# Kernel tuning notes

Measured on AMD Instinct MI355X. Metric: run time of the kernel, lower is better.

Reference implementation:

```python
import jax, jax.numpy as jnp
import numpy as np
import math

B, S, E, H = 2, 2048, 1024, 16
D = E // H  # d_head = 64

def setup_inputs() -> dict:
    key = jax.random.key(0)
    ks = jax.random.split(key, 7)
    query = jax.random.normal(ks[0], (B, S, E), dtype=jnp.float32)
    k_in = jax.random.normal(ks[1], (B, S, E), dtype=jnp.float32)
    v_in = jax.random.normal(ks[2], (B, S, E), dtype=jnp.float32)
    # causal mask, broadcastable over batch and heads; mask==0 positions are blocked
    mask = jnp.tril(jnp.ones((S, S), dtype=jnp.int32))[None, None]
    scale = 1.0 / math.sqrt(E)
    w_q = jax.random.normal(ks[3], (E, E), dtype=jnp.float32) * scale
    w_k = jax.random.normal(ks[4], (E, E), dtype=jnp.float32) * scale
    w_v = jax.random.normal(ks[5], (E, E), dtype=jnp.float32) * scale
    w_o = jax.random.normal(ks[6], (E, E), dtype=jnp.float32) * scale
    return {"query": query, "key": k_in, "value": v_in, "mask": mask,
            "w_q": w_q, "w_k": w_k, "w_v": w_v, "w_o": w_o}

def reference(query, key, value, mask, w_q, w_k, w_v, w_o):
    # projections (nn.Linear with no bias: x @ W^T); split heads -> [B,H,S,D]
    q = (query @ w_q.T).reshape(B, S, H, D).transpose(0, 2, 1, 3)
    k = (key @ w_k.T).reshape(B, S, H, D).transpose(0, 2, 1, 3)
    v = (value @ w_v.T).reshape(B, S, H, D).transpose(0, 2, 1, 3)
    # scaled dot-product scores [B,H,S,S]
    scores = jnp.einsum('bhqd,bhkd->bhqk', q, k) / math.sqrt(D)
    scores = jnp.where(mask == 0, jnp.float32(-1e9), scores)
    attn = jax.nn.softmax(scores, axis=-1)  # dropout p=0.0 -> identity
    out = jnp.einsum('bhqk,bhkd->bhqd', attn, v)  # [B,H,S,D]
    out = out.transpose(0, 2, 1, 3).reshape(B, S, E)
    return out @ w_o.T
```

## Files before the change

### kernel.cpp

```cpp
#include <hip/hip_runtime.h>
#include <hip/hip_bf16.h>

#define B_ 2
#define S_ 2048
#define E_ 1024
#define H_ 16
#define D_ 64

typedef __attribute__((ext_vector_type(8))) short bf16x8;
typedef __attribute__((ext_vector_type(4))) float f32x4;

static __device__ __forceinline__ unsigned short f2bf(float x) {
    union { float f; unsigned u; } v; v.f = x;
    unsigned r = v.u + 0x7FFF + ((v.u >> 16) & 1);
    return (unsigned short)(r >> 16);
}

static __device__ __forceinline__ unsigned pack2bf(float a, float b) {
    union { float f; unsigned u; } x, y; x.f = a; y.f = b;
    unsigned ra = x.u + 0x7FFF + ((x.u >> 16) & 1);
    unsigned rb = y.u + 0x7FFF + ((y.u >> 16) & 1);
    return (ra >> 16) | (rb & 0xFFFF0000u);
}

static __device__ __forceinline__ unsigned packtrunc(float a, float b) {
    union { float f; unsigned u; } x, y; x.f = a; y.f = b;
    return __builtin_amdgcn_perm(y.u, x.u, 0x07060302);
}

static __device__ __forceinline__ void async_copy16(const void* gsrc, void* ldst) {
    __builtin_amdgcn_global_load_lds(
        (const __attribute__((address_space(1))) void*)gsrc,
        (__attribute__((address_space(3))) void*)ldst, 16, 0, 0);
}

__global__ void cvt_multi(const float* __restrict__ s0, const float* __restrict__ s1,
                          const float* __restrict__ s2, const float* __restrict__ s3,
                          unsigned short* __restrict__ dst, int n4,
                          float c0, float c1, float c2, float c3) {
    const float* src = (blockIdx.y == 0) ? s0 : (blockIdx.y == 1) ? s1
                     : (blockIdx.y == 2) ? s2 : s3;
    float c = (blockIdx.y == 0) ? c0 : (blockIdx.y == 1) ? c1
            : (blockIdx.y == 2) ? c2 : c3;
    int i = blockIdx.x * blockDim.x + threadIdx.x;
    if (i >= n4) return;
    float4 f = ((const float4*)src)[i];
    ushort4 o;
    o.x = f2bf(f.x * c); o.y = f2bf(f.y * c); o.z = f2bf(f.z * c); o.w = f2bf(f.w * c);
    ((ushort4*)(dst + (size_t)blockIdx.y * n4 * 4))[i] = o;
}

template <int MODE>
__global__ __launch_bounds__(256) void gemm128(
    const unsigned short* __restrict__ A0, const unsigned short* __restrict__ B0,
    void* __restrict__ C0, int M, int N, int K) {
    __shared__ __align__(16) unsigned short Al[2][128 * 64];
    __shared__ __align__(16) unsigned short Bl[2][128 * 64];
    const unsigned short* A = A0;
    const unsigned short* Bm = B0;
    int z = 0;
    if (MODE == 4) {
        z = blockIdx.z;
        A  = A0 + (size_t)z * 4194304;
        Bm = B0 + (size_t)z * 1048576;
    }
    const int bm = blockIdx.y * 128, bn = blockIdx.x * 128;
    const int tid = threadIdx.x;
    const int w = tid >> 6, lane = tid & 63;
    const int col = lane & 15, quad = lane >> 4, swz = col & 7;
    const int wm = (w >> 1) * 64, wn = (w & 1) * 64;

    f32x4 acc[4][4] = {};

#pragma unroll
    for (int it = 0; it < 4; it++) {
        int s = tid + it * 256, r = s >> 3, cg = (s & 7) ^ (r & 7);
        async_copy16(A + (size_t)(bm + r) * K + cg * 8, &Al[0][s * 8]);
        async_copy16(Bm + (size_t)(bn + r) * K + cg * 8, &Bl[0][s * 8]);
    }

    const int nk = K >> 6;
    for (int kt = 0; kt < nk; kt++) {
        const int cur = kt & 1;
        __syncthreads();
        if (kt + 1 < nk) {
            const int k1 = (kt + 1) << 6, nb = cur ^ 1;
#pragma unroll
            for (int it = 0; it < 4; it++) {
                int s = tid + it * 256, r = s >> 3, cg = (s & 7) ^ (r & 7);
                async_copy16(A + (size_t)(bm + r) * K + k1 + cg * 8, &Al[nb][s * 8]);
                async_copy16(Bm + (size_t)(bn + r) * K + k1 + cg * 8, &Bl[nb][s * 8]);
            }
        }
        const unsigned short* Ab = &Al[cur][0];
        const unsigned short* Bb = &Bl[cur][0];
#pragma unroll
        for (int h = 0; h < 2; h++) {
            const int cq = ((h * 4 + quad) ^ swz) * 8;
            bf16x8 af[4], bf[4];
#pragma unroll
            for (int i = 0; i < 4; i++) af[i] = *(const bf16x8*)&Ab[(wm + i * 16 + col) * 64 + cq];
#pragma unroll
            for (int j = 0; j < 4; j++) bf[j] = *(const bf16x8*)&Bb[(wn + j * 16 + col) * 64 + cq];
#pragma unroll
            for (int i = 0; i < 4; i++)
#pragma unroll
                for (int j = 0; j < 4; j++)
                    acc[i][j] = __builtin_amdgcn_mfma_f32_16x16x32_bf16(af[i], bf[j], acc[i][j], 0, 0, 0);
        }
    }

    if (MODE == 3) {
#pragma unroll
        for (int i = 0; i < 4; i++)
#pragma unroll
            for (int j = 0; j < 4; j++)
#pragma unroll
                for (int r = 0; r < 4; r++) {
                    int gm = bm + wm + i * 16 + quad * 4 + r;
                    int gn = bn + wn + j * 16 + col;
                    ((float*)C0)[(size_t)gm * N + gn] = acc[i][j][r];
                }
    } else {
        __syncthreads();
        unsigned short* scr = ((w < 2) ? &Al[0][0] : &Bl[0][0]) + (w & 1) * 4096;
        const int b  = (bm + wm) >> 11;
        const int s0 = (bm + wm) & 2047;
        const int hh = (bn + wn) >> 6;
        unsigned short* outp = (unsigned short*)C0 + (size_t)z * 4194304;
        if (z == 2) {
#pragma unroll
            for (int i = 0; i < 4; i++)
#pragma unroll
                for (int j = 0; j < 4; j++) {
                    int n = j * 16 + col;
                    int c = i * 2 + (quad >> 1);
                    uint2 pk;
                    pk.x = pack2bf(acc[i][j][0], acc[i][j][1]);
                    pk.y = pack2bf(acc[i][j][2], acc[i][j][3]);
                    *(uint2*)&scr[n * 64 + ((c ^ (n & 7)) << 3) + ((quad & 1) << 2)] = pk;
                }
#pragma unroll
            for (int it = 0; it < 8; it++) {
                int slot = it * 64 + lane, n = slot >> 3, c = slot & 7;
                uint4 v = *(uint4*)&scr[n * 64 + ((c ^ (n & 7)) << 3)];
                *(uint4*)&outp[(((size_t)b * H_ + hh) * D_ + n) * S_ + s0 + c * 8] = v;
            }
        } else {
#pragma unroll
            for (int i = 0; i < 4; i++)
#pragma unroll
                for (int j = 0; j < 4; j++)
#pragma unroll
                    for (int r = 0; r < 4; r++) {
                        int m = i * 16 + quad * 4 + r, n = j * 16 + col;
                        scr[m * 64 + (((n >> 3) ^ (m & 7)) << 3) + (n & 7)] = f2bf(acc[i][j][r]);
                    }
#pragma unroll
            for (int it = 0; it < 8; it++) {
                int slot = it * 64 + lane, m = slot >> 3, c = slot & 7;
                uint4 v = *(uint4*)&scr[m * 64 + ((c ^ (m & 7)) << 3)];
                *(uint4*)&outp[(((size_t)b * H_ + hh) * S_ + s0 + m) * (size_t)D_ + c * 8] = v;
            }
        }
    }
}

__global__ __launch_bounds__(512) void attn_kernel(
    const unsigned short* __restrict__ Q, const unsigned short* __restrict__ K_,
    const unsigned short* __restrict__ Vt, unsigned short* __restrict__ Out) {
    __shared__ __align__(16) unsigned short KV[4][4096];
    __shared__ __align__(16) float Lred[4][2][64];
    const int bh = blockIdx.y;
    const int qb = (bh >= 16) ? (int)blockIdx.x : 15 - (int)blockIdx.x;
    const int q0 = qb * 128;
    const int tid = threadIdx.x;
    const int w = tid >> 6, lane = tid & 63;
    const int qg = w >> 1, kh = w & 1, kh32 = kh << 5;
    const int col = lane & 15, quad = lane >> 4, swz = col & 7;
    const int qw0 = q0 + qg * 32;
    const float NINF = -__builtin_huge_valf();

    const unsigned short* Qh = Q + (size_t)bh * S_ * D_;
    const unsigned short* Kh = K_ + (size_t)bh * S_ * D_;
    const unsigned short* Vh = Vt + (size_t)bh * D_ * S_;

    bf16x8 qf[2][2];
#pragma unroll
    for (int i = 0; i < 2; i++)
#pragma unroll
        for (int h = 0; h < 2; h++)
            qf[i][h] = *(const bf16x8*)(Qh + (size_t)(qw0 + i * 16 + col) * 64 + h * 32 + quad * 8);

    f32x4 o[2][4] = {};
    float lsum[2] = {0.f, 0.f};

    {
        int s = tid, r = s >> 3, cg = (s & 7) ^ (r & 7);
        async_copy16(Kh + (size_t)r * 64 + cg * 8, &KV[0][s * 8]);
        async_copy16(Vh + (size_t)r * S_ + cg * 8, &KV[2][s * 8]);
    }

    const int nk = 2 * (qb + 1);
    for (int kt = 0; kt < nk; kt++) {
        const int k0 = kt * 64;
        const int cur = kt & 1;
        __syncthreads();
        if (kt + 1 < nk) {
            const int k1 = k0 + 64, nb = cur ^ 1;
            int s = tid, r = s >> 3, cg = (s & 7) ^ (r & 7);
            async_copy16(Kh + (size_t)(k1 + r) * 64 + cg * 8, &KV[nb][s * 8]);
            async_copy16(Vh + (size_t)r * S_ + k1 + cg * 8, &KV[2 + nb][s * 8]);
        }
        if (k0 + kh32 > qw0 + 31) continue;

        const unsigned short* Kb = &KV[cur][0];
        const unsigned short* Vb = &KV[2 + cur][0];

        f32x4 sc[2][2] = {};
#pragma unroll
        for (int h = 0; h < 2; h++) {
            const int cq = ((h * 4 + quad) ^ swz) * 8;
#pragma unroll
            for (int ct = 0; ct < 2; ct++) {
                bf16x8 kf = *(const bf16x8*)&Kb[(kh32 + ct * 16 + col) * 64 + cq];
                sc[0][ct] = __builtin_amdgcn_mfma_f32_16x16x32_bf16(kf, qf[0][h], sc[0][ct], 0, 0, 0);
                sc[1][ct] = __builtin_amdgcn_mfma_f32_16x16x32_bf16(kf, qf[1][h], sc[1][ct], 0, 0, 0);
            }
        }
        if (k0 + kh32 + 31 <= qw0) {
#pragma unroll
            for (int i = 0; i < 2; i++)
#pragma unroll
                for (int ct = 0; ct < 2; ct++) {
#pragma unroll
                    for (int r = 0; r < 4; r++)
                        sc[i][ct][r] = __builtin_amdgcn_exp2f(sc[i][ct][r]);
                    lsum[i] += (sc[i][ct][0] + sc[i][ct][1]) + (sc[i][ct][2] + sc[i][ct][3]);
                }
        } else {
#pragma unroll
            for (int i = 0; i < 2; i++)
#pragma unroll
                for (int ct = 0; ct < 2; ct++) {
#pragma unroll
                    for (int r = 0; r < 4; r++) {
                        int key = k0 + kh32 + ct * 16 + quad * 4 + r;
                        int qi = qw0 + i * 16 + col;
                        float s = (key <= qi) ? sc[i][ct][r] : NINF;
                        sc[i][ct][r] = __builtin_amdgcn_exp2f(s);
                    }
                    lsum[i] += (sc[i][ct][0] + sc[i][ct][1]) + (sc[i][ct][2] + sc[i][ct][3]);
                }
        }
        union { bf16x8 v; unsigned u[4]; } pf[2];
#pragma unroll
        for (int i = 0; i < 2; i++) {
            pf[i].u[0] = packtrunc(sc[i][0][0], sc[i][0][1]);
            pf[i].u[1] = packtrunc(sc[i][0][2], sc[i][0][3]);
            pf[i].u[2] = packtrunc(sc[i][1][0], sc[i][1][1]);
            pf[i].u[3] = packtrunc(sc[i][1][2], sc[i][1][3]);
        }
#pragma unroll
        for (int dt = 0; dt < 4; dt++) {
            const int row = dt * 16 + col;
            const int ko0 = kh32 + quad * 4;
            const int ko1 = ko0 + 16;
            union { bf16x8 v; uint2 d2[2]; } vf;
            vf.d2[0] = *(const uint2*)&Vb[row * 64 + (((ko0 >> 3) ^ (row & 7)) << 3) + (ko0 & 7)];
            vf.d2[1] = *(const uint2*)&Vb[row * 64 + (((ko1 >> 3) ^ (row & 7)) << 3) + (ko1 & 7)];
#pragma unroll
            for (int i = 0; i < 2; i++)
                o[i][dt] = __builtin_amdgcn_mfma_f32_16x16x32_bf16(vf.v, pf[i].v, o[i][dt], 0, 0, 0);
        }
    }

    __syncthreads();
    if (kh == 1) {
        f32x4* R = (f32x4*)&KV[0][0] + qg * 512 + lane * 8;
#pragma unroll
        for (int i = 0; i < 2; i++)
#pragma unroll
            for (int dt = 0; dt < 4; dt++) R[i * 4 + dt] = o[i][dt];
        Lred[qg][0][lane] = lsum[0];
        Lred[qg][1][lane] = lsum[1];
    }
    __syncthreads();
    if (kh == 0) {
        f32x4* R = (f32x4*)&KV[0][0] + qg * 512 + lane * 8;
#pragma unroll
        for (int i = 0; i < 2; i++)
#pragma unroll
            for (int dt = 0; dt < 4; dt++) o[i][dt] += R[i * 4 + dt];
        lsum[0] += Lred[qg][0][lane];
        lsum[1] += Lred[qg][1][lane];

        const int b = bh >> 4, hh = bh & 15;
#pragma unroll
        for (int i = 0; i < 2; i++) {
            float l = lsum[i];
            l += __shfl_xor(l, 16);
            l += __shfl_xor(l, 32);
            float inv = 1.f / l;
            int gq = qw0 + i * 16 + col;
#pragma unroll
            for (int dt = 0; dt < 4; dt++) {
                uint2 pk;
                pk.x = pack2bf(o[i][dt][0] * inv, o[i][dt][1] * inv);
                pk.y = pack2bf(o[i][dt][2] * inv, o[i][dt][3] * inv);
                *(uint2*)&Out[((size_t)b * S_ + gq) * E_ + hh * 64 + dt * 16 + quad * 4] = pk;
            }
        }
    }
}

extern "C" void kernel_launch(void* const* d_in, const int* in_sizes, int n_in,
                              void* d_out, int out_size, void* d_ws, size_t ws_size,
                              hipStream_t stream) {
    const float* query = (const float*)d_in[0];
    const float* key_i = (const float*)d_in[1];
    const float* value = (const float*)d_in[2];
    const float* w_q = (const float*)d_in[4];
    const float* w_k = (const float*)d_in[5];
    const float* w_v = (const float*)d_in[6];
    const float* w_o = (const float*)d_in[7];
    float* out = (float*)d_out;

    const int M = B_ * S_;
    const int N = E_, K = E_;
    const size_t nX = (size_t)M * E_;
    const size_t nW = (size_t)E_ * E_;

    char* ws = (char*)d_ws;
    unsigned short* xq  = (unsigned short*)(ws);
    unsigned short* wqb = (unsigned short*)(ws + (24u << 20));
    unsigned short* Qb  = (unsigned short*)(ws + (32u << 20));
    unsigned short* Kb  = (unsigned short*)(ws + (40u << 20));
    unsigned short* Vtb = (unsigned short*)(ws + (48u << 20));
    unsigned short* Ab  = (unsigned short*)(ws + (56u << 20));

    const float SCQ = 0.125f * 1.44269504088896f;

    int n4x = (int)(nX / 4), n4w = (int)(nW / 4);
    cvt_multi<<<dim3((n4x + 255) / 256, 3), 256, 0, stream>>>(
        query, key_i, value, value, xq, n4x, 1.f, 1.f, 1.f, 1.f);
    cvt_multi<<<dim3((n4w + 255) / 256, 4), 256, 0, stream>>>(
        w_q, w_k, w_v, w_o, wqb, n4w, SCQ, 1.f, 1.f, 1.f);

    gemm128<4><<<dim3(N / 128, M / 128, 3), 256, 0, stream>>>(xq, wqb, Qb, M, N, K);

    attn_kernel<<<dim3(S_ / 128, B_ * H_), 512, 0, stream>>>(Qb, Kb, Vtb, Ab);

    gemm128<3><<<dim3(N / 128, M / 128), 256, 0, stream>>>(
        Ab, wqb + 3u * 1048576u, out, M, N, K);
}
```

Before: 226.5 us.

## Merge conversion kernels and remap block order for XCD-aware L2 locality

```diff
diff --git a/kernel.cpp b/kernel.cpp
--- a/kernel.cpp
+++ b/kernel.cpp
@@ -34,20 +34,30 @@
         (__attribute__((address_space(3))) void*)ldst, 16, 0, 0);
 }
 
-__global__ void cvt_multi(const float* __restrict__ s0, const float* __restrict__ s1,
-                          const float* __restrict__ s2, const float* __restrict__ s3,
-                          unsigned short* __restrict__ dst, int n4,
-                          float c0, float c1, float c2, float c3) {
-    const float* src = (blockIdx.y == 0) ? s0 : (blockIdx.y == 1) ? s1
-                     : (blockIdx.y == 2) ? s2 : s3;
-    float c = (blockIdx.y == 0) ? c0 : (blockIdx.y == 1) ? c1
-            : (blockIdx.y == 2) ? c2 : c3;
-    int i = blockIdx.x * blockDim.x + threadIdx.x;
-    if (i >= n4) return;
+__global__ void cvt_all(const float* __restrict__ s0, const float* __restrict__ s1,
+                        const float* __restrict__ s2, const float* __restrict__ s3,
+                        const float* __restrict__ s4, const float* __restrict__ s5,
+                        const float* __restrict__ s6,
+                        unsigned short* __restrict__ xdst, unsigned short* __restrict__ wdst,
+                        float scq) {
+    int b = blockIdx.x;
+    const float* src; unsigned short* dst; int i; float c = 1.f;
+    if (b < 12288) {
+        int ti = b >> 12, lb = b & 4095;
+        src = (ti == 0) ? s0 : (ti == 1) ? s1 : s2;
+        dst = xdst + (size_t)ti * 4194304;
+        i = lb * 256 + threadIdx.x;
+    } else {
+        int r = b - 12288, ti = r >> 10, lb = r & 1023;
+        src = (ti == 0) ? s3 : (ti == 1) ? s4 : (ti == 2) ? s5 : s6;
+        dst = wdst + (size_t)ti * 1048576;
+        i = lb * 256 + threadIdx.x;
+        if (ti == 0) c = scq;
+    }
     float4 f = ((const float4*)src)[i];
     ushort4 o;
     o.x = f2bf(f.x * c); o.y = f2bf(f.y * c); o.z = f2bf(f.z * c); o.w = f2bf(f.w * c);
-    ((ushort4*)(dst + (size_t)blockIdx.y * n4 * 4))[i] = o;
+    ((ushort4*)dst)[i] = o;
 }
 
 template <int MODE>
@@ -64,7 +74,10 @@
         A  = A0 + (size_t)z * 4194304;
         Bm = B0 + (size_t)z * 1048576;
     }
-    const int bm = blockIdx.y * 128, bn = blockIdx.x * 128;
+    const int o = (int)(blockIdx.x + (blockIdx.y << 3));
+    const int cx = o & 7, tx = o >> 3;
+    const int bm = ((cx << 2) + (tx >> 3)) * 128;
+    const int bn = (tx & 7) * 128;
     const int tid = threadIdx.x;
     const int w = tid >> 6, lane = tid & 63;
     const int col = lane & 15, quad = lane >> 4, swz = col & 7;
@@ -171,8 +184,11 @@
     const unsigned short* __restrict__ Vt, unsigned short* __restrict__ Out) {
     __shared__ __align__(16) unsigned short KV[4][4096];
     __shared__ __align__(16) float Lred[4][2][64];
-    const int bh = blockIdx.y;
-    const int qb = (bh >= 16) ? (int)blockIdx.x : 15 - (int)blockIdx.x;
+    const int o = (int)(blockIdx.x + (blockIdx.y << 4));
+    const int cx = o & 7, tx = o >> 3;
+    const int bh = (cx << 2) + (tx & 3);
+    const int qi = tx >> 2;
+    const int qb = (bh >= 16) ? qi : 15 - qi;
     const int q0 = qb * 128;
     const int tid = threadIdx.x;
     const int w = tid >> 6, lane = tid & 63;
@@ -192,7 +208,7 @@
         for (int h = 0; h < 2; h++)
             qf[i][h] = *(const bf16x8*)(Qh + (size_t)(qw0 + i * 16 + col) * 64 + h * 32 + quad * 8);
 
-    f32x4 o[2][4] = {};
+    f32x4 o_[2][4] = {};
     float lsum[2] = {0.f, 0.f};
 
     {
@@ -246,8 +262,8 @@
 #pragma unroll
                     for (int r = 0; r < 4; r++) {
                         int key = k0 + kh32 + ct * 16 + quad * 4 + r;
-                        int qi = qw0 + i * 16 + col;
-                        float s = (key <= qi) ? sc[i][ct][r] : NINF;
+                        int qidx = qw0 + i * 16 + col;
+                        float s = (key <= qidx) ? sc[i][ct][r] : NINF;
                         sc[i][ct][r] = __builtin_amdgcn_exp2f(s);
                     }
                     lsum[i] += (sc[i][ct][0] + sc[i][ct][1]) + (sc[i][ct][2] + sc[i][ct][3]);
@@ -271,7 +287,7 @@
             vf.d2[1] = *(const uint2*)&Vb[row * 64 + (((ko1 >> 3) ^ (row & 7)) << 3) + (ko1 & 7)];
 #pragma unroll
             for (int i = 0; i < 2; i++)
-                o[i][dt] = __builtin_amdgcn_mfma_f32_16x16x32_bf16(vf.v, pf[i].v, o[i][dt], 0, 0, 0);
+                o_[i][dt] = __builtin_amdgcn_mfma_f32_16x16x32_bf16(vf.v, pf[i].v, o_[i][dt], 0, 0, 0);
         }
     }
 
@@ -281,7 +297,7 @@
 #pragma unroll
         for (int i = 0; i < 2; i++)
 #pragma unroll
-            for (int dt = 0; dt < 4; dt++) R[i * 4 + dt] = o[i][dt];
+            for (int dt = 0; dt < 4; dt++) R[i * 4 + dt] = o_[i][dt];
         Lred[qg][0][lane] = lsum[0];
         Lred[qg][1][lane] = lsum[1];
     }
@@ -291,7 +307,7 @@
 #pragma unroll
         for (int i = 0; i < 2; i++)
 #pragma unroll
-            for (int dt = 0; dt < 4; dt++) o[i][dt] += R[i * 4 + dt];
+            for (int dt = 0; dt < 4; dt++) o_[i][dt] += R[i * 4 + dt];
         lsum[0] += Lred[qg][0][lane];
         lsum[1] += Lred[qg][1][lane];
 
@@ -306,8 +322,8 @@
 #pragma unroll
             for (int dt = 0; dt < 4; dt++) {
                 uint2 pk;
-                pk.x = pack2bf(o[i][dt][0] * inv, o[i][dt][1] * inv);
-                pk.y = pack2bf(o[i][dt][2] * inv, o[i][dt][3] * inv);
+                pk.x = pack2bf(o_[i][dt][0] * inv, o_[i][dt][1] * inv);
+                pk.y = pack2bf(o_[i][dt][2] * inv, o_[i][dt][3] * inv);
                 *(uint2*)&Out[((size_t)b * S_ + gq) * E_ + hh * 64 + dt * 16 + quad * 4] = pk;
             }
         }
@@ -328,8 +344,6 @@
 
     const int M = B_ * S_;
     const int N = E_, K = E_;
-    const size_t nX = (size_t)M * E_;
-    const size_t nW = (size_t)E_ * E_;
 
     char* ws = (char*)d_ws;
     unsigned short* xq  = (unsigned short*)(ws);
@@ -341,11 +355,8 @@
 
     const float SCQ = 0.125f * 1.44269504088896f;
 
-    int n4x = (int)(nX / 4), n4w = (int)(nW / 4);
-    cvt_multi<<<dim3((n4x + 255) / 256, 3), 256, 0, stream>>>(
-        query, key_i, value, value, xq, n4x, 1.f, 1.f, 1.f, 1.f);
-    cvt_multi<<<dim3((n4w + 255) / 256, 4), 256, 0, stream>>>(
-        w_q, w_k, w_v, w_o, wqb, n4w, SCQ, 1.f, 1.f, 1.f);
+    cvt_all<<<16384, 256, 0, stream>>>(query, key_i, value, w_q, w_k, w_v, w_o,
+                                       xq, wqb, SCQ);
 
     gemm128<4><<<dim3(N / 128, M / 128, 3), 256, 0, stream>>>(xq, wqb, Qb, M, N, K);
 
```

After: 219.1 us. 3.3% less time.
